# Kernel tuning notes

Measured on AMD Instinct MI355X. Metric: run time of the kernel, lower is better.

The kernel has to match this reference:

```python
import math
import jax, jax.numpy as jnp
import numpy as np

B, S, HID = 1, 2048, 4096
NH, NKV, D = 32, 8, 128
THETA = 10000.0


def setup_inputs() -> dict:
    key = jax.random.key(0)
    k1, k2, k3, k4, k5 = jax.random.split(key, 5)
    hidden_states = jax.random.normal(k1, (B, S, HID), dtype=jnp.float32)
    k_cache = jax.random.normal(k2, (B, NKV, S, D), dtype=jnp.float32)
    v_cache = jax.random.normal(k3, (B, NKV, S, D), dtype=jnp.float32)
    Wq = jax.random.normal(k4, (HID, NH * D), dtype=jnp.float32) * 0.02
    Wo = jax.random.normal(k5, (NH * D, HID), dtype=jnp.float32) * 0.02
    position_ids = jnp.broadcast_to(jnp.arange(S, dtype=jnp.int32), (B, S))
    # causal mask: True = masked out (torch.where(mask, -10000, scores))
    attention_mask = jnp.broadcast_to(
        jnp.triu(jnp.ones((S, S), dtype=bool), k=1)[None, None], (B, 1, S, S)
    )
    return {
        "hidden_states": hidden_states,
        "k_cache": k_cache,
        "v_cache": v_cache,
        "Wq": Wq,
        "Wo": Wo,
        "position_ids": position_ids,
        "attention_mask": attention_mask,
    }


def _rotate_half(x):
    x1, x2 = jnp.split(x, 2, axis=-1)
    return jnp.concatenate([-x2, x1], axis=-1)


def _rope_tables(position_ids):
    # Llama rotary embedding gathered at position_ids -> [B, 1, S, D]
    inv_freq = 1.0 / (THETA ** (jnp.arange(0, D, 2, dtype=jnp.float32) / D))
    freqs = position_ids[..., None].astype(jnp.float32) * inv_freq  # [B, S, D/2]
    emb = jnp.concatenate([freqs, freqs], axis=-1)  # [B, S, D]
    return jnp.cos(emb)[:, None], jnp.sin(emb)[:, None]


def reference(hidden_states, k_cache, v_cache, Wq, Wo, position_ids, attention_mask):
    G = NH // NKV  # GQA group size
    # q projection: [B, S, HID] -> [B, NH, S, D]
    q = (hidden_states @ Wq).reshape(B, S, NH, D).transpose(0, 2, 1, 3)
    cos, sin = _rope_tables(position_ids)
    q = q * cos + _rotate_half(q) * sin
    # GQA without materializing repeat_kv: group query heads over kv heads
    qg = q.reshape(B, NKV, G, S, D)
    scores = jnp.einsum("bkgsd,bktd->bkgst", qg, k_cache) / math.sqrt(D)
    scores = scores.reshape(B, NH, S, S)
    scores = jnp.where(attention_mask, jnp.float32(-10000.0), scores)
    probs = jax.nn.softmax(scores.astype(jnp.float32), axis=-1).astype(q.dtype)
    out = jnp.einsum("bkgst,bktd->bkgsd", probs.reshape(B, NKV, G, S, S), v_cache)
    out = out.reshape(B, NH, S, D).transpose(0, 2, 1, 3).reshape(B, S, NH * D)
    return out @ Wo
```

## Files before the change

kernel.cpp:

```cpp
#include <hip/hip_runtime.h>
#include <cstdint>
#include <cstddef>

#define S_LEN 2048
#define HID 4096
#define NH 32
#define NKV 8
#define HD 128

typedef __attribute__((ext_vector_type(4))) float f32x4;
typedef __attribute__((ext_vector_type(8))) short bf16x8;

__device__ __forceinline__ unsigned short f2bf(float f) {
  union { float f; uint32_t u; } v; v.f = f;
  uint32_t r = v.u + 0x7FFFu + ((v.u >> 16) & 1u);
  return (unsigned short)(r >> 16);
}

__device__ __forceinline__ float exp2_fast(float x) {
#if __has_builtin(__builtin_amdgcn_exp2f)
  return __builtin_amdgcn_exp2f(x);
#else
  float r; asm("v_exp_f32 %0, %1" : "=v"(r) : "v"(x)); return r;
#endif
}

__device__ __forceinline__ unsigned int cvt_pk_bf16(float lo, float hi) {
  unsigned int r;
  asm("v_cvt_pk_bf16_f32 %0, %1, %2" : "=v"(r) : "v"(lo), "v"(hi));
  return r;
}

__global__ void cvt_bf16_kernel(const float* __restrict__ in,
                                unsigned short* __restrict__ out, int n4) {
  int i = blockIdx.x * blockDim.x + threadIdx.x;
  if (i >= n4) return;
  float4 v = ((const float4*)in)[i];
  ushort4 o;
  o.x = f2bf(v.x); o.y = f2bf(v.y); o.z = f2bf(v.z); o.w = f2bf(v.w);
  ((ushort4*)out)[i] = o;
}

__global__ __launch_bounds__(256) void transpose_cvt2_kernel(
    const float* __restrict__ in0, unsigned short* __restrict__ out0,
    const float* __restrict__ in1, unsigned short* __restrict__ out1,
    int R, int C) {
  __shared__ float tile[64][65];
  const float* inb = (blockIdx.z == 0) ? in0 : in1;
  unsigned short* outb = (blockIdx.z == 0) ? out0 : out1;
  const int c0 = blockIdx.x * 64, r0 = blockIdx.y * 64;
  const int tid = threadIdx.x;
#pragma unroll
  for (int p = 0; p < 4; ++p) {
    const int ch = p * 256 + tid;
    const int r = ch >> 4, off = (ch & 15) << 2;
    *(float4*)&tile[r][off] = *(const float4*)(inb + (size_t)(r0 + r) * C + c0 + off);
  }
  __syncthreads();
#pragma unroll
  for (int p = 0; p < 2; ++p) {
    const int ch = p * 256 + tid;
    const int i = ch >> 3, j0 = (ch & 7) << 3;
    bf16x8 v;
#pragma unroll
    for (int k = 0; k < 8; ++k) v[k] = (short)f2bf(tile[j0 + k][i]);
    *(bf16x8*)(outb + (size_t)(c0 + i) * R + r0 + j0) = v;
  }
}

__global__ __launch_bounds__(256) void transpose_cvt_kernel(
    const float* __restrict__ in, unsigned short* __restrict__ out, int R, int C) {
  __shared__ float tile[64][65];
  const int b = blockIdx.z;
  const float* inb = in + (size_t)b * R * C;
  unsigned short* outb = out + (size_t)b * R * C;
  const int c0 = blockIdx.x * 64, r0 = blockIdx.y * 64;
  const int tid = threadIdx.x;
#pragma unroll
  for (int p = 0; p < 4; ++p) {
    const int ch = p * 256 + tid;
    const int r = ch >> 4, off = (ch & 15) << 2;
    *(float4*)&tile[r][off] = *(const float4*)(inb + (size_t)(r0 + r) * C + c0 + off);
  }
  __syncthreads();
#pragma unroll
  for (int p = 0; p < 2; ++p) {
    const int ch = p * 256 + tid;
    const int i = ch >> 3, j0 = (ch & 7) << 3;
    bf16x8 v;
#pragma unroll
    for (int k = 0; k < 8; ++k) v[k] = (short)f2bf(tile[j0 + k][i]);
    *(bf16x8*)(outb + (size_t)(c0 + i) * R + r0 + j0) = v;
  }
}

__global__ __launch_bounds__(256, 2) void gemm_bt_kernel(
    const unsigned short* __restrict__ A, const unsigned short* __restrict__ BT,
    float* __restrict__ C, int M, int N, int K) {
  __shared__ __align__(16) unsigned short As[2][128 * 64];
  __shared__ __align__(16) unsigned short Bs[2][128 * 64];
  const int tid = threadIdx.x;
  const int lane = tid & 63;
  const int wid = tid >> 6;
  const int wm = (wid >> 1) * 64, wn = (wid & 1) * 64;
  const int g = blockIdx.x;
  const int xcd = g & 7, local = g >> 3;
  const int m0 = (xcd * 2 + (local & 1)) * 128;
  const int n0 = (local >> 1) * 128;
  const int lr = lane & 15;
  const int quad = lane >> 4;
  const int sw = lr & 7;
  const int nkt = K >> 6;

  auto stage = [&](int buf, int kt) {
#pragma unroll
    for (int p = 0; p < 4; ++p) {
      const int c = p * 256 + tid;
      const int r = c >> 3, jsrc = (c & 7) ^ (r & 7);
      __builtin_amdgcn_global_load_lds(
          (const __attribute__((address_space(1))) void*)(A + (size_t)(m0 + r) * K + kt * 64 + jsrc * 8),
          (__attribute__((address_space(3))) void*)(&As[buf][c * 8]), 16, 0, 0);
      __builtin_amdgcn_global_load_lds(
          (const __attribute__((address_space(1))) void*)(BT + (size_t)(n0 + r) * K + kt * 64 + jsrc * 8),
          (__attribute__((address_space(3))) void*)(&Bs[buf][c * 8]), 16, 0, 0);
    }
  };

  f32x4 acc[4][4] = {};
  stage(0, 0);
  __syncthreads();
  int bufv = 0;
  for (int t = 0; t < nkt; ++t) {
    if (t + 1 < nkt) stage(bufv ^ 1, t + 1);
    const unsigned short* as = As[bufv];
    const unsigned short* bs = Bs[bufv];
#pragma unroll
    for (int h = 0; h < 2; ++h) {
      const int pos = ((h * 4 + quad) ^ sw) << 3;
      bf16x8 a[4], b[4];
#pragma unroll
      for (int tq = 0; tq < 4; ++tq) {
        a[tq] = *(const bf16x8*)(as + (wm + tq * 16 + lr) * 64 + pos);
        b[tq] = *(const bf16x8*)(bs + (wn + tq * 16 + lr) * 64 + pos);
      }
#pragma unroll
      for (int mt = 0; mt < 4; ++mt)
#pragma unroll
        for (int nt = 0; nt < 4; ++nt)
          acc[mt][nt] = __builtin_amdgcn_mfma_f32_16x16x32_bf16(a[mt], b[nt], acc[mt][nt], 0, 0, 0);
    }
    __syncthreads();
    bufv ^= 1;
  }
  const int qd = quad << 2;
#pragma unroll
  for (int mt = 0; mt < 4; ++mt)
#pragma unroll
    for (int nt = 0; nt < 4; ++nt) {
      const int row = m0 + wm + mt * 16 + qd;
      const int col = n0 + wn + nt * 16 + lr;
#pragma unroll
      for (int r = 0; r < 4; ++r)
        C[(size_t)(row + r) * N + col] = acc[mt][nt][r];
    }
}

__global__ __launch_bounds__(256, 2) void gemm_rope_kernel(
    const unsigned short* __restrict__ A, const unsigned short* __restrict__ BT,
    const int* __restrict__ pos_ids, unsigned short* __restrict__ Qout) {
  __shared__ __align__(16) unsigned short As[2][128 * 64];
  __shared__ __align__(16) unsigned short Bs[2][128 * 64];
  const int tid = threadIdx.x;
  const int lane = tid & 63;
  const int wid = tid >> 6;
  const int wm = wid * 32;
  const int g = blockIdx.x;
  const int xcd = g & 7, local = g >> 3;
  const int m0 = (xcd * 2 + (local & 1)) * 128;
  const int n0 = (local >> 1) * 128;
  const int lr = lane & 15;
  const int quad = lane >> 4;
  const int sw = lr & 7;
  const int nkt = HID >> 6;

  auto stage = [&](int buf, int kt) {
#pragma unroll
    for (int p = 0; p < 4; ++p) {
      const int c = p * 256 + tid;
      const int r = c >> 3, jsrc = (c & 7) ^ (r & 7);
      __builtin_amdgcn_global_load_lds(
          (const __attribute__((address_space(1))) void*)(A + (size_t)(m0 + r) * HID + kt * 64 + jsrc * 8),
          (__attribute__((address_space(3))) void*)(&As[buf][c * 8]), 16, 0, 0);
      __builtin_amdgcn_global_load_lds(
          (const __attribute__((address_space(1))) void*)(BT + (size_t)(n0 + r) * HID + kt * 64 + jsrc * 8),
          (__attribute__((address_space(3))) void*)(&Bs[buf][c * 8]), 16, 0, 0);
    }
  };

  f32x4 acc[2][8] = {};
  stage(0, 0);
  __syncthreads();
  int bufv = 0;
  for (int t = 0; t < nkt; ++t) {
    if (t + 1 < nkt) stage(bufv ^ 1, t + 1);
    const unsigned short* as = As[bufv];
    const unsigned short* bs = Bs[bufv];
#pragma unroll
    for (int h = 0; h < 2; ++h) {
      const int pos = ((h * 4 + quad) ^ sw) << 3;
      bf16x8 a[2], b[8];
#pragma unroll
      for (int tq = 0; tq < 2; ++tq)
        a[tq] = *(const bf16x8*)(as + (wm + tq * 16 + lr) * 64 + pos);
#pragma unroll
      for (int tq = 0; tq < 8; ++tq)
        b[tq] = *(const bf16x8*)(bs + (tq * 16 + lr) * 64 + pos);
#pragma unroll
      for (int mt = 0; mt < 2; ++mt)
#pragma unroll
        for (int nt = 0; nt < 8; ++nt)
          acc[mt][nt] = __builtin_amdgcn_mfma_f32_16x16x32_bf16(a[mt], b[nt], acc[mt][nt], 0, 0, 0);
    }
    __syncthreads();
    bufv ^= 1;
  }
  const int qd = quad << 2;
  const int h = n0 >> 7;
#pragma unroll
  for (int mt = 0; mt < 2; ++mt)
#pragma unroll
    for (int r = 0; r < 4; ++r) {
      const int row = m0 + wm + mt * 16 + qd + r;
      const float pos = (float)pos_ids[row];
#pragma unroll
      for (int nt = 0; nt < 4; ++nt) {
        const int i = nt * 16 + lr;
        const float invf = __expf(-(float)(2 * i) * (9.2103403719761836f / 128.0f));
        float sn, cs;
        __sincosf(pos * invf, &sn, &cs);
        const float x1 = acc[mt][nt][r], x2 = acc[mt][nt + 4][r];
        Qout[((size_t)h * S_LEN + row) * HD + i]      = f2bf(x1 * cs - x2 * sn);
        Qout[((size_t)h * S_LEN + row) * HD + i + 64] = f2bf(x2 * cs + x1 * sn);
      }
    }
}

__global__ __launch_bounds__(256, 2) void attn_kernel(
    const unsigned short* __restrict__ Q, const unsigned short* __restrict__ Kc,
    const unsigned short* __restrict__ VT, unsigned short* __restrict__ Aout) {
  __shared__ __align__(16) unsigned short Ks[64 * 136];
  __shared__ __align__(16) unsigned short Vs[128 * 72];
  __shared__ __align__(16) unsigned short Ps[128 * 72];
  const int tid = threadIdx.x, lane = tid & 63, wid = tid >> 6;
  const int qh = blockIdx.x;
  const int qt = (blockIdx.y < 8) ? (15 - (int)blockIdx.y) : ((int)blockIdx.y - 8);
  const int kvh = qh >> 2;
  const int lr = lane & 15, quad = lane >> 4;
  const float SC = 0.12751619754705767f;
  const float NB = -23.083120654223414f;

  bf16x8 qf[2][4];
#pragma unroll
  for (int mt = 0; mt < 2; ++mt)
#pragma unroll
    for (int kk = 0; kk < 4; ++kk)
      qf[mt][kk] = *(const bf16x8*)(Q + ((size_t)qh * S_LEN + qt * 128 + wid * 32 + mt * 16 + lr) * HD + kk * 32 + quad * 8);

  f32x4 o[2][8] = {};
  float lsum[2] = {0.f, 0.f};

  const int prow0 = (wid * 32 + lr) * 72;
  const int nkt = 2 * qt + 2;
  for (int kt2 = 0; kt2 < nkt; ++kt2) {
    bf16x8 kr[4], vr[4];
#pragma unroll
    for (int p = 0; p < 4; ++p) {
      const int c = p * 256 + tid;
      kr[p] = *(const bf16x8*)(Kc + ((size_t)kvh * S_LEN + kt2 * 64 + (c >> 4)) * HD + (c & 15) * 8);
      vr[p] = *(const bf16x8*)(VT + ((size_t)kvh * HD + (c >> 3)) * S_LEN + kt2 * 64 + (c & 7) * 8);
    }
    __syncthreads();
#pragma unroll
    for (int p = 0; p < 4; ++p) {
      const int c = p * 256 + tid;
      *(bf16x8*)(Ks + (c >> 4) * 136 + (c & 15) * 8) = kr[p];
      *(bf16x8*)(Vs + (c >> 3) * 72 + (c & 7) * 8) = vr[p];
    }
    __syncthreads();

    const bool dtile = (kt2 >= 2 * qt);
#pragma unroll
    for (int nt = 0; nt < 4; ++nt) {
      f32x4 s0 = {}, s1 = {};
#pragma unroll
      for (int kk = 0; kk < 4; ++kk) {
        bf16x8 kf = *(const bf16x8*)(Ks + (nt * 16 + lr) * 136 + kk * 32 + quad * 8);
        s0 = __builtin_amdgcn_mfma_f32_16x16x32_bf16(kf, qf[0][kk], s0, 0, 0, 0);
        s1 = __builtin_amdgcn_mfma_f32_16x16x32_bf16(kf, qf[1][kk], s1, 0, 0, 0);
      }
      const int skey0 = kt2 * 64 + nt * 16 + quad * 4;
#pragma unroll
      for (int mt = 0; mt < 2; ++mt) {
        const f32x4 s = mt ? s1 : s0;
        const int qrow = qt * 128 + wid * 32 + mt * 16 + lr;
        float pv[4];
        float ls = 0.f;
#pragma unroll
        for (int r = 0; r < 4; ++r) {
          float v = fmaf(s[r], SC, NB);
          if (dtile && (skey0 + r) > qrow) v = -1e30f;
          pv[r] = exp2_fast(v);
          ls += pv[r];
        }
        lsum[mt] += ls;
        uint2 pk;
        pk.x = cvt_pk_bf16(pv[0], pv[1]);
        pk.y = cvt_pk_bf16(pv[2], pv[3]);
        *(uint2*)(Ps + prow0 + mt * 16 * 72 + nt * 16 + quad * 4) = pk;
      }
    }
    bf16x8 pf[2][2];
#pragma unroll
    for (int mt = 0; mt < 2; ++mt)
#pragma unroll
      for (int kk = 0; kk < 2; ++kk)
        pf[mt][kk] = *(const bf16x8*)(Ps + prow0 + mt * 16 * 72 + kk * 32 + quad * 8);
#pragma unroll
    for (int dt = 0; dt < 8; ++dt)
#pragma unroll
      for (int kk = 0; kk < 2; ++kk) {
        bf16x8 vf = *(const bf16x8*)(Vs + (dt * 16 + lr) * 72 + kk * 32 + quad * 8);
        o[0][dt] = __builtin_amdgcn_mfma_f32_16x16x32_bf16(vf, pf[0][kk], o[0][dt], 0, 0, 0);
        o[1][dt] = __builtin_amdgcn_mfma_f32_16x16x32_bf16(vf, pf[1][kk], o[1][dt], 0, 0, 0);
      }
  }

#pragma unroll
  for (int mt = 0; mt < 2; ++mt) {
    float l = lsum[mt];
    l += __shfl_xor(l, 16);
    l += __shfl_xor(l, 32);
    const float inv = 1.0f / l;
    const int qrow = qt * 128 + wid * 32 + mt * 16 + lr;
#pragma unroll
    for (int dt = 0; dt < 8; ++dt) {
      uint2 w;
      w.x = cvt_pk_bf16(o[mt][dt][0] * inv, o[mt][dt][1] * inv);
      w.y = cvt_pk_bf16(o[mt][dt][2] * inv, o[mt][dt][3] * inv);
      *(uint2*)(Aout + (size_t)qrow * HID + qh * HD + dt * 16 + quad * 4) = w;
    }
  }
}

extern "C" void kernel_launch(void* const* d_in, const int* in_sizes, int n_in,
                              void* d_out, int out_size, void* d_ws, size_t ws_size,
                              hipStream_t stream) {
  const float* hidden  = (const float*)d_in[0];
  const float* k_cache = (const float*)d_in[1];
  const float* v_cache = (const float*)d_in[2];
  const float* Wq      = (const float*)d_in[3];
  const float* Wo      = (const float*)d_in[4];
  const int*   pos     = (const int*)d_in[5];
  float* out = (float*)d_out;

  char* ws = (char*)d_ws;
  unsigned short* hidden_bf = (unsigned short*)(ws + 0);
  unsigned short* attn_bf   = hidden_bf;
  unsigned short* WqT       = (unsigned short*)(ws + 16777216);
  unsigned short* WoT       = (unsigned short*)(ws + 50331648);
  unsigned short* k_bf      = (unsigned short*)(ws + 83886080);
  unsigned short* vT        = (unsigned short*)(ws + 88080384);
  unsigned short* q_bf      = (unsigned short*)(ws + 92274688);

  cvt_bf16_kernel<<<(S_LEN * HID / 4 + 255) / 256, 256, 0, stream>>>(hidden, hidden_bf, S_LEN * HID / 4);
  cvt_bf16_kernel<<<(NKV * S_LEN * HD / 4 + 255) / 256, 256, 0, stream>>>(k_cache, k_bf, NKV * S_LEN * HD / 4);
  transpose_cvt2_kernel<<<dim3(HID / 64, HID / 64, 2), 256, 0, stream>>>(Wq, WqT, Wo, WoT, HID, HID);
  transpose_cvt_kernel<<<dim3(HD / 64, S_LEN / 64, NKV), 256, 0, stream>>>(v_cache, vT, S_LEN, HD);

  gemm_rope_kernel<<<dim3((S_LEN / 128) * (HID / 128)), 256, 0, stream>>>(hidden_bf, WqT, pos, q_bf);
  attn_kernel<<<dim3(NH, S_LEN / 128), 256, 0, stream>>>(q_bf, k_bf, vT, attn_bf);
  gemm_bt_kernel<<<dim3((S_LEN / 128) * (HID / 128)), 256, 0, stream>>>(attn_bf, WoT, out, S_LEN, HID, HID);
}
```

Baseline: 422.0 us.

## Merge preprocessing launches, use 2x2 warp tiling in QK GEMM, swizzle attention LDS

Folds the two fp32-to-bf16 conversion launches into one kernel, and the weight and V-cache transposes into a single 3-slice grid, cutting launch count from four to two. The Q-projection GEMM moves from 4x1 warps, each covering 32 rows by all 128 columns, to 2x2 warps of 64x64 with interleaved column tiles so each warp still holds the RoPE pairs. This changes the LDS read mix per warp. Attention's K, V and P shared tiles drop their padding in favour of XOR swizzling, which shrinks LDS use and aims to avoid bank conflicts. The risk is wasted blocks in the z=2 slice, which exit early, and possible new conflicts from the swizzle pattern.

```diff
diff --git a/kernel.cpp b/kernel.cpp
--- a/kernel.cpp
+++ b/kernel.cpp
@@ -31,50 +31,44 @@
   return r;
 }
 
-__global__ void cvt_bf16_kernel(const float* __restrict__ in,
-                                unsigned short* __restrict__ out, int n4) {
-  int i = blockIdx.x * blockDim.x + threadIdx.x;
-  if (i >= n4) return;
-  float4 v = ((const float4*)in)[i];
+__global__ void cvt2_bf16_kernel(const float* __restrict__ hidden,
+                                 unsigned short* __restrict__ hidden_bf,
+                                 const float* __restrict__ k_cache,
+                                 unsigned short* __restrict__ k_bf) {
+  const int i = blockIdx.x * blockDim.x + threadIdx.x;
+  const float* in;
+  unsigned short* out;
+  int j;
+  if (i < 2097152) { in = hidden; out = hidden_bf; j = i; }
+  else             { in = k_cache; out = k_bf; j = i - 2097152; }
+  float4 v = ((const float4*)in)[j];
   ushort4 o;
   o.x = f2bf(v.x); o.y = f2bf(v.y); o.z = f2bf(v.z); o.w = f2bf(v.w);
-  ((ushort4*)out)[i] = o;
-}
-
-__global__ __launch_bounds__(256) void transpose_cvt2_kernel(
-    const float* __restrict__ in0, unsigned short* __restrict__ out0,
-    const float* __restrict__ in1, unsigned short* __restrict__ out1,
-    int R, int C) {
+  ((ushort4*)out)[j] = o;
+}
+
+__global__ __launch_bounds__(256) void transpose_cvt3_kernel(
+    const float* __restrict__ Wq, unsigned short* __restrict__ WqT,
+    const float* __restrict__ Wo, unsigned short* __restrict__ WoT,
+    const float* __restrict__ v_cache, unsigned short* __restrict__ vT) {
   __shared__ float tile[64][65];
-  const float* inb = (blockIdx.z == 0) ? in0 : in1;
-  unsigned short* outb = (blockIdx.z == 0) ? out0 : out1;
-  const int c0 = blockIdx.x * 64, r0 = blockIdx.y * 64;
-  const int tid = threadIdx.x;
-#pragma unroll
-  for (int p = 0; p < 4; ++p) {
-    const int ch = p * 256 + tid;
-    const int r = ch >> 4, off = (ch & 15) << 2;
-    *(float4*)&tile[r][off] = *(const float4*)(inb + (size_t)(r0 + r) * C + c0 + off);
-  }
-  __syncthreads();
-#pragma unroll
-  for (int p = 0; p < 2; ++p) {
-    const int ch = p * 256 + tid;
-    const int i = ch >> 3, j0 = (ch & 7) << 3;
-    bf16x8 v;
-#pragma unroll
-    for (int k = 0; k < 8; ++k) v[k] = (short)f2bf(tile[j0 + k][i]);
-    *(bf16x8*)(outb + (size_t)(c0 + i) * R + r0 + j0) = v;
-  }
-}
-
-__global__ __launch_bounds__(256) void transpose_cvt_kernel(
-    const float* __restrict__ in, unsigned short* __restrict__ out, int R, int C) {
-  __shared__ float tile[64][65];
-  const int b = blockIdx.z;
-  const float* inb = in + (size_t)b * R * C;
-  unsigned short* outb = out + (size_t)b * R * C;
-  const int c0 = blockIdx.x * 64, r0 = blockIdx.y * 64;
+  const float* inb;
+  unsigned short* outb;
+  int R, C, c0, r0;
+  if (blockIdx.z < 2) {
+    inb = blockIdx.z ? Wo : Wq;
+    outb = blockIdx.z ? WoT : WqT;
+    R = HID; C = HID;
+    c0 = blockIdx.x * 64; r0 = blockIdx.y * 64;
+  } else {
+    const int id = blockIdx.y * 64 + blockIdx.x;
+    if (id >= 512) return;
+    const int hd = id >> 6, rem = id & 63;
+    inb = v_cache + (size_t)hd * S_LEN * HD;
+    outb = vT + (size_t)hd * S_LEN * HD;
+    R = S_LEN; C = HD;
+    c0 = (rem & 1) * 64; r0 = (rem >> 1) * 64;
+  }
   const int tid = threadIdx.x;
 #pragma unroll
   for (int p = 0; p < 4; ++p) {
@@ -173,7 +167,8 @@
   const int tid = threadIdx.x;
   const int lane = tid & 63;
   const int wid = tid >> 6;
-  const int wm = wid * 32;
+  const int jn = wid & 1;
+  const int wm = (wid >> 1) * 64;
   const int g = blockIdx.x;
   const int xcd = g & 7, local = g >> 3;
   const int m0 = (xcd * 2 + (local & 1)) * 128;
@@ -197,7 +192,7 @@
     }
   };
 
-  f32x4 acc[2][8] = {};
+  f32x4 acc[4][4] = {};
   stage(0, 0);
   __syncthreads();
   int bufv = 0;
@@ -208,17 +203,16 @@
 #pragma unroll
     for (int h = 0; h < 2; ++h) {
       const int pos = ((h * 4 + quad) ^ sw) << 3;
-      bf16x8 a[2], b[8];
-#pragma unroll
-      for (int tq = 0; tq < 2; ++tq)
+      bf16x8 a[4], b[4];
+#pragma unroll
+      for (int tq = 0; tq < 4; ++tq) {
         a[tq] = *(const bf16x8*)(as + (wm + tq * 16 + lr) * 64 + pos);
-#pragma unroll
-      for (int tq = 0; tq < 8; ++tq)
-        b[tq] = *(const bf16x8*)(bs + (tq * 16 + lr) * 64 + pos);
-#pragma unroll
-      for (int mt = 0; mt < 2; ++mt)
-#pragma unroll
-        for (int nt = 0; nt < 8; ++nt)
+        b[tq] = *(const bf16x8*)(bs + ((jn + 2 * tq) * 16 + lr) * 64 + pos);
+      }
+#pragma unroll
+      for (int mt = 0; mt < 4; ++mt)
+#pragma unroll
+        for (int nt = 0; nt < 4; ++nt)
           acc[mt][nt] = __builtin_amdgcn_mfma_f32_16x16x32_bf16(a[mt], b[nt], acc[mt][nt], 0, 0, 0);
     }
     __syncthreads();
@@ -227,18 +221,18 @@
   const int qd = quad << 2;
   const int h = n0 >> 7;
 #pragma unroll
-  for (int mt = 0; mt < 2; ++mt)
+  for (int mt = 0; mt < 4; ++mt)
 #pragma unroll
     for (int r = 0; r < 4; ++r) {
       const int row = m0 + wm + mt * 16 + qd + r;
       const float pos = (float)pos_ids[row];
 #pragma unroll
-      for (int nt = 0; nt < 4; ++nt) {
-        const int i = nt * 16 + lr;
+      for (int t = 0; t < 2; ++t) {
+        const int i = (jn + 2 * t) * 16 + lr;
         const float invf = __expf(-(float)(2 * i) * (9.2103403719761836f / 128.0f));
         float sn, cs;
         __sincosf(pos * invf, &sn, &cs);
-        const float x1 = acc[mt][nt][r], x2 = acc[mt][nt + 4][r];
+        const float x1 = acc[mt][t][r], x2 = acc[mt][t + 2][r];
         Qout[((size_t)h * S_LEN + row) * HD + i]      = f2bf(x1 * cs - x2 * sn);
         Qout[((size_t)h * S_LEN + row) * HD + i + 64] = f2bf(x2 * cs + x1 * sn);
       }
@@ -248,14 +242,15 @@
 __global__ __launch_bounds__(256, 2) void attn_kernel(
     const unsigned short* __restrict__ Q, const unsigned short* __restrict__ Kc,
     const unsigned short* __restrict__ VT, unsigned short* __restrict__ Aout) {
-  __shared__ __align__(16) unsigned short Ks[64 * 136];
-  __shared__ __align__(16) unsigned short Vs[128 * 72];
-  __shared__ __align__(16) unsigned short Ps[128 * 72];
+  __shared__ __align__(16) unsigned short Ks[64 * 128];
+  __shared__ __align__(16) unsigned short Vs[128 * 64];
+  __shared__ __align__(16) unsigned short Ps[128 * 64];
   const int tid = threadIdx.x, lane = tid & 63, wid = tid >> 6;
   const int qh = blockIdx.x;
   const int qt = (blockIdx.y < 8) ? (15 - (int)blockIdx.y) : ((int)blockIdx.y - 8);
   const int kvh = qh >> 2;
   const int lr = lane & 15, quad = lane >> 4;
+  const int sw7 = lr & 7;
   const float SC = 0.12751619754705767f;
   const float NB = -23.083120654223414f;
 
@@ -269,7 +264,7 @@
   f32x4 o[2][8] = {};
   float lsum[2] = {0.f, 0.f};
 
-  const int prow0 = (wid * 32 + lr) * 72;
+  const int prow0 = (wid * 32 + lr) * 64;
   const int nkt = 2 * qt + 2;
   for (int kt2 = 0; kt2 < nkt; ++kt2) {
     bf16x8 kr[4], vr[4];
@@ -283,8 +278,10 @@
 #pragma unroll
     for (int p = 0; p < 4; ++p) {
       const int c = p * 256 + tid;
-      *(bf16x8*)(Ks + (c >> 4) * 136 + (c & 15) * 8) = kr[p];
-      *(bf16x8*)(Vs + (c >> 3) * 72 + (c & 7) * 8) = vr[p];
+      const int krow = c >> 4, kch = (c & 15) ^ (krow & 7);
+      *(bf16x8*)(Ks + krow * 128 + kch * 8) = kr[p];
+      const int vrow = c >> 3, vch = (c & 7) ^ (vrow & 7);
+      *(bf16x8*)(Vs + vrow * 64 + vch * 8) = vr[p];
     }
     __syncthreads();
 
@@ -294,7 +291,7 @@
       f32x4 s0 = {}, s1 = {};
 #pragma unroll
       for (int kk = 0; kk < 4; ++kk) {
-        bf16x8 kf = *(const bf16x8*)(Ks + (nt * 16 + lr) * 136 + kk * 32 + quad * 8);
+        bf16x8 kf = *(const bf16x8*)(Ks + (nt * 16 + lr) * 128 + (((kk * 4 + quad) ^ sw7) << 3));
         s0 = __builtin_amdgcn_mfma_f32_16x16x32_bf16(kf, qf[0][kk], s0, 0, 0, 0);
         s1 = __builtin_amdgcn_mfma_f32_16x16x32_bf16(kf, qf[1][kk], s1, 0, 0, 0);
       }
@@ -316,7 +313,8 @@
         uint2 pk;
         pk.x = cvt_pk_bf16(pv[0], pv[1]);
         pk.y = cvt_pk_bf16(pv[2], pv[3]);
-        *(uint2*)(Ps + prow0 + mt * 16 * 72 + nt * 16 + quad * 4) = pk;
+        *(uint2*)(Ps + prow0 + mt * 16 * 64 +
+                  ((((2 * nt + (quad >> 1)) ^ sw7) << 3) + ((quad & 1) << 2))) = pk;
       }
     }
     bf16x8 pf[2][2];
@@ -324,12 +322,12 @@
     for (int mt = 0; mt < 2; ++mt)
 #pragma unroll
       for (int kk = 0; kk < 2; ++kk)
-        pf[mt][kk] = *(const bf16x8*)(Ps + prow0 + mt * 16 * 72 + kk * 32 + quad * 8);
+        pf[mt][kk] = *(const bf16x8*)(Ps + prow0 + mt * 16 * 64 + (((kk * 4 + quad) ^ sw7) << 3));
 #pragma unroll
     for (int dt = 0; dt < 8; ++dt)
 #pragma unroll
       for (int kk = 0; kk < 2; ++kk) {
-        bf16x8 vf = *(const bf16x8*)(Vs + (dt * 16 + lr) * 72 + kk * 32 + quad * 8);
+        bf16x8 vf = *(const bf16x8*)(Vs + (dt * 16 + lr) * 64 + (((kk * 4 + quad) ^ sw7) << 3));
         o[0][dt] = __builtin_amdgcn_mfma_f32_16x16x32_bf16(vf, pf[0][kk], o[0][dt], 0, 0, 0);
         o[1][dt] = __builtin_amdgcn_mfma_f32_16x16x32_bf16(vf, pf[1][kk], o[1][dt], 0, 0, 0);
       }
@@ -372,10 +370,8 @@
   unsigned short* vT        = (unsigned short*)(ws + 88080384);
   unsigned short* q_bf      = (unsigned short*)(ws + 92274688);
 
-  cvt_bf16_kernel<<<(S_LEN * HID / 4 + 255) / 256, 256, 0, stream>>>(hidden, hidden_bf, S_LEN * HID / 4);
-  cvt_bf16_kernel<<<(NKV * S_LEN * HD / 4 + 255) / 256, 256, 0, stream>>>(k_cache, k_bf, NKV * S_LEN * HD / 4);
-  transpose_cvt2_kernel<<<dim3(HID / 64, HID / 64, 2), 256, 0, stream>>>(Wq, WqT, Wo, WoT, HID, HID);
-  transpose_cvt_kernel<<<dim3(HD / 64, S_LEN / 64, NKV), 256, 0, stream>>>(v_cache, vT, S_LEN, HD);
+  cvt2_bf16_kernel<<<10240, 256, 0, stream>>>(hidden, hidden_bf, k_cache, k_bf);
+  transpose_cvt3_kernel<<<dim3(64, 64, 3), 256, 0, stream>>>(Wq, WqT, Wo, WoT, v_cache, vT);
 
   gemm_rope_kernel<<<dim3((S_LEN / 128) * (HID / 128)), 256, 0, stream>>>(hidden_bf, WqT, pos, q_bf);
   attn_kernel<<<dim3(NH, S_LEN / 128), 256, 0, stream>>>(q_bf, k_bf, vT, attn_bf);
```

Result: faster. 412.8 us (-2.2%).
